# Kernel tuning notes

Measured on AMD Instinct MI355X. Metric: run time of the kernel, lower is better.

Reference implementation:

```python
import jax, jax.numpy as jnp
import numpy as np

N_NODES = 100000
N_EDGES = 1600000
HIDDEN = 64
N_MID = 3  # num_layers=5 -> 1 first + 3 middle + 1 last


def setup_inputs() -> dict:
    key = jax.random.key(0)
    ks = jax.random.split(key, 12)
    x = jax.random.normal(ks[0], (N_NODES, 1), dtype=jnp.float32)
    edge_index = jax.random.randint(ks[1], (2, N_EDGES), 0, N_NODES, dtype=jnp.int32)
    edge_weight = jax.random.uniform(ks[2], (N_EDGES,), dtype=jnp.float32)
    s0 = 1.0  # fan_in=1
    sh = 1.0 / np.sqrt(HIDDEN)
    Wrel0 = jax.random.normal(ks[3], (HIDDEN, 1), dtype=jnp.float32) * s0
    brel0 = jax.random.normal(ks[4], (HIDDEN,), dtype=jnp.float32) * s0
    Wroot0 = jax.random.normal(ks[5], (HIDDEN, 1), dtype=jnp.float32) * s0
    Wrel_mid = jax.random.normal(ks[6], (N_MID, HIDDEN, HIDDEN), dtype=jnp.float32) * sh
    brel_mid = jax.random.normal(ks[7], (N_MID, HIDDEN), dtype=jnp.float32) * sh
    Wroot_mid = jax.random.normal(ks[8], (N_MID, HIDDEN, HIDDEN), dtype=jnp.float32) * sh
    WrelL = jax.random.normal(ks[9], (1, HIDDEN), dtype=jnp.float32) * sh
    brelL = jax.random.normal(ks[10], (1,), dtype=jnp.float32) * sh
    WrootL = jax.random.normal(ks[11], (1, HIDDEN), dtype=jnp.float32) * sh
    return {"x": x, "edge_index": edge_index, "edge_weight": edge_weight,
            "Wrel0": Wrel0, "brel0": brel0, "Wroot0": Wroot0,
            "Wrel_mid": Wrel_mid, "brel_mid": brel_mid, "Wroot_mid": Wroot_mid,
            "WrelL": WrelL, "brelL": brelL, "WrootL": WrootL}


def reference(x, edge_index, edge_weight, Wrel0, brel0, Wroot0,
              Wrel_mid, brel_mid, Wroot_mid, WrelL, brelL, WrootL):
    src = edge_index[0]
    dst = edge_index[1]
    n = x.shape[0]

    def conv(h, Wrel, brel, Wroot):
        # PyG GraphConv(aggr='add'): lin_rel(sum_j w_ij * h_j) + lin_root(h_i)
        msg = h[src] * edge_weight[:, None]          # [E, C]
        agg = jax.ops.segment_sum(msg, dst, num_segments=n)  # [N, C]
        return agg @ Wrel.T + brel + h @ Wroot.T

    # dropout omitted (deterministic reference); relu after all but last layer
    h = jax.nn.relu(conv(x, Wrel0, brel0, Wroot0))
    for i in range(Wrel_mid.shape[0]):
        h = jax.nn.relu(conv(h, Wrel_mid[i], brel_mid[i], Wroot_mid[i]))
    return conv(h, WrelL, brelL, WrootL)  # [N, 1]
```

## Files before the change

kernel.cpp:

```cpp
#include <hip/hip_runtime.h>
#include <stdint.h>


#define NN 100000
#define NE 1600000
#define HID 64
#define NBKT 391
#define CAP 8192
#define TILE 4096
#define EPT 16
#define NTILE ((NE + TILE - 1) / TILE)
#define CHUNK 32

typedef __attribute__((ext_vector_type(8))) short bf16x8;
typedef __attribute__((ext_vector_type(4))) float f32x4;

__device__ __forceinline__ uint32_t rne_bf16(float v) {
    uint32_t u = __float_as_uint(v);
    return (u + 0x7fffu + ((u >> 16) & 1u)) >> 16;
}


__global__ __launch_bounds__(256) void k_bpart(const int* __restrict__ src,
                                               const int* __restrict__ dst,
                                               const float* __restrict__ w,
                                               int* __restrict__ bcur,
                                               int2* __restrict__ bpairs) {
    __shared__ int  hcnt[NBKT];
    __shared__ int  hoff[NBKT];
    __shared__ int  hadj[NBKT];
    __shared__ int  sc0[512];
    __shared__ int  sc1[512];
    __shared__ int2 sT[TILE];
    __shared__ int  sAdj[TILE];
    int tile0 = blockIdx.x * TILE;
    int t = threadIdx.x;
    for (int i = t; i < NBKT; i += 256) hcnt[i] = 0;
    __syncthreads();

    int   pk[EPT];
    int   bk[EPT];
    float wv[EPT];
    #pragma unroll
    for (int k = 0; k < EPT; k++) {
        int e = tile0 + t + k * 256;
        if (e < NE) {
            int d = dst[e];
            int b = d >> 8;
            pk[k] = (src[e] << 8) | (d & 255);
            wv[k] = w[e];
            bk[k] = b;
            atomicAdd(&hcnt[b], 1);
        } else {
            bk[k] = -1;
        }
    }
    __syncthreads();

    sc0[t]       = (t < NBKT) ? hcnt[t] : 0;
    sc0[t + 256] = (t + 256 < NBKT) ? hcnt[t + 256] : 0;
    __syncthreads();
    int* cur = sc0;
    int* oth = sc1;
    for (int off = 1; off < 512; off <<= 1) {
        int v0 = cur[t]       + ((t       >= off) ? cur[t - off]       : 0);
        int v1 = cur[t + 256] + ((t + 256 >= off) ? cur[t + 256 - off] : 0);
        oth[t] = v0;
        oth[t + 256] = v1;
        __syncthreads();
        int* tmp = cur; cur = oth; oth = tmp;
    }
    for (int i = t; i < NBKT; i += 256) {
        int c = hcnt[i];
        int excl = cur[i] - c;
        hoff[i] = excl;
        int gbase = c ? atomicAdd(&bcur[i], c) : 0;
        hadj[i] = gbase - excl;
        hcnt[i] = 0;
    }
    __syncthreads();

    #pragma unroll
    for (int k = 0; k < EPT; k++) {
        if (bk[k] >= 0) {
            int b = bk[k];
            int pos = hoff[b] + atomicAdd(&hcnt[b], 1);
            sT[pos] = make_int2(pk[k], __float_as_int(wv[k]));
            sAdj[pos] = hadj[b];
        }
    }
    __syncthreads();

    int n = NE - tile0; if (n > TILE) n = TILE;
    for (int j = t; j < n; j += 256)
        bpairs[sAdj[j] + j] = sT[j];
}

__global__ __launch_bounds__(256) void k_bcsr(const int* __restrict__ bcur,
                                              const int2* __restrict__ bpairs,
                                              int* __restrict__ offs,
                                              int* __restrict__ ends,
                                              uint32_t* __restrict__ pairs) {
    __shared__ int2 sE[CAP];
    __shared__ int cnt[256];
    __shared__ int scn[256];
    __shared__ int cur[256];
    int k = blockIdx.x, t = threadIdx.x;
    int base = k * CAP;
    int scnt = bcur[k] - base;
    cnt[t] = 0;
    __syncthreads();
    for (int j = t; j < scnt; j += 256) {
        int2 q = bpairs[base + j];
        sE[j] = q;
        atomicAdd(&cnt[q.x & 255], 1);
    }
    __syncthreads();
    int v = cnt[t], acc = v;
    scn[t] = v;
    __syncthreads();
    for (int off = 1; off < 256; off <<= 1) {
        int u = (t >= off) ? scn[t - off] : 0;
        __syncthreads();
        acc += u;
        scn[t] = acc;
        __syncthreads();
    }
    int excl = acc - v;
    cur[t] = excl;
    int d = (k << 8) + t;
    if (d < NN) {
        offs[d] = base + excl;
        ends[d] = base + excl + v;
    }
    __syncthreads();
    for (int j = t; j < scnt; j += 256) {
        int2 q = sE[j];
        int pos = base + atomicAdd(&cur[q.x & 255], 1);
        uint32_t wb = rne_bf16(__int_as_float(q.y)) & 0x7fffu;
        pairs[pos] = (wb << 17) | (uint32_t)(q.x >> 8);
    }
}


__global__ __launch_bounds__(256) void k_wsplit(const float* __restrict__ Wrel_mid,
                                                const float* __restrict__ Wroot_mid,
                                                uint16_t* __restrict__ WgH,
                                                uint16_t* __restrict__ WgL,
                                                uint16_t* __restrict__ WrH,
                                                uint16_t* __restrict__ WrL,
                                                int* __restrict__ bcur) {
    int i = blockIdx.x * blockDim.x + threadIdx.x;
    if (i < NBKT) bcur[i] = i * CAP;
    if (i >= 3 * 4096) return;
    float a = Wrel_mid[i];
    uint32_t ah = rne_bf16(a);
    float al = a - __uint_as_float(ah << 16);
    WgH[i] = (uint16_t)ah;
    WgL[i] = (uint16_t)rne_bf16(al);
    float b = Wroot_mid[i];
    uint32_t bh = rne_bf16(b);
    float bl = b - __uint_as_float(bh << 16);
    WrH[i] = (uint16_t)bh;
    WrL[i] = (uint16_t)rne_bf16(bl);
}


__device__ __forceinline__ void mfma_epilogue(
        int lane, int w, const uint32_t* sH,
        const uint16_t* __restrict__ WgH, const uint16_t* __restrict__ WgL,
        const uint16_t* __restrict__ WrH, const uint16_t* __restrict__ WrL,
        const float* __restrict__ brel,
        uint16_t* sG, uint16_t* sR) {
    int row = lane & 15;
    int quad = lane >> 4;
    int kb = quad * 8;
    bf16x8 ah0 = *(const bf16x8*)&sH[row * 36 + quad * 4];
    bf16x8 ah1 = *(const bf16x8*)&sH[row * 36 + 16 + quad * 4];
    int oc = w * 16 + row;
    {
        bf16x8 bh0 = *(const bf16x8*)&WgH[oc * 64 + kb];
        bf16x8 bh1 = *(const bf16x8*)&WgH[oc * 64 + 32 + kb];
        bf16x8 bl0 = *(const bf16x8*)&WgL[oc * 64 + kb];
        bf16x8 bl1 = *(const bf16x8*)&WgL[oc * 64 + 32 + kb];
        f32x4 acc = {0.f, 0.f, 0.f, 0.f};
        acc = __builtin_amdgcn_mfma_f32_16x16x32_bf16(ah0, bh0, acc, 0, 0, 0);
        acc = __builtin_amdgcn_mfma_f32_16x16x32_bf16(ah1, bh1, acc, 0, 0, 0);
        acc = __builtin_amdgcn_mfma_f32_16x16x32_bf16(ah0, bl0, acc, 0, 0, 0);
        acc = __builtin_amdgcn_mfma_f32_16x16x32_bf16(ah1, bl1, acc, 0, 0, 0);
        #pragma unroll
        for (int r = 0; r < 4; r++)
            sG[(quad * 4 + r) * 68 + oc] = (uint16_t)rne_bf16(acc[r]);
    }
    {
        bf16x8 bh0 = *(const bf16x8*)&WrH[oc * 64 + kb];
        bf16x8 bh1 = *(const bf16x8*)&WrH[oc * 64 + 32 + kb];
        bf16x8 bl0 = *(const bf16x8*)&WrL[oc * 64 + kb];
        bf16x8 bl1 = *(const bf16x8*)&WrL[oc * 64 + 32 + kb];
        float bias = brel[oc];
        f32x4 acc = {bias, bias, bias, bias};
        acc = __builtin_amdgcn_mfma_f32_16x16x32_bf16(ah0, bh0, acc, 0, 0, 0);
        acc = __builtin_amdgcn_mfma_f32_16x16x32_bf16(ah1, bh1, acc, 0, 0, 0);
        acc = __builtin_amdgcn_mfma_f32_16x16x32_bf16(ah0, bl0, acc, 0, 0, 0);
        acc = __builtin_amdgcn_mfma_f32_16x16x32_bf16(ah1, bl1, acc, 0, 0, 0);
        #pragma unroll
        for (int r = 0; r < 4; r++)
            sR[(quad * 4 + r) * 68 + oc] = (uint16_t)rne_bf16(acc[r]);
    }
}

__device__ __forceinline__ void epilogue_writeout(
        int tid, int blk16, const uint16_t* sG, const uint16_t* sR,
        uint16_t* __restrict__ Gout, uint16_t* __restrict__ Rout) {
    const uint32_t* sGd = (const uint32_t*)sG;
    const uint32_t* sRd = (const uint32_t*)sR;
    uint32_t* Gd = (uint32_t*)Gout;
    uint32_t* Rd = (uint32_t*)Rout;
    #pragma unroll
    for (int it = 0; it < 2; it++) {
        int idx = it * 256 + tid;
        int nd = idx >> 5, col = idx & 31;
        Gd[(blk16 + nd) * 32 + col] = sGd[nd * 34 + col];
        Rd[(blk16 + nd) * 32 + col] = sRd[nd * 34 + col];
    }
}


__global__ __launch_bounds__(256) void k_l0pre(
        const int* __restrict__ offs, const int* __restrict__ ends,
        const uint32_t* __restrict__ pairs, const float* __restrict__ x,
        const float* __restrict__ Wrel0, const float* __restrict__ brel0,
        const float* __restrict__ Wroot0,
        const uint16_t* __restrict__ WgH, const uint16_t* __restrict__ WgL,
        const uint16_t* __restrict__ WrH, const uint16_t* __restrict__ WrL,
        const float* __restrict__ brel,
        uint16_t* __restrict__ Gout, uint16_t* __restrict__ Rout) {
    __shared__ uint32_t sH[16 * 36];
    __shared__ uint16_t sG[16 * 68];
    __shared__ uint16_t sR[16 * 68];
    int c = threadIdx.x & 63;
    int w = threadIdx.x >> 6;
    int blk16 = blockIdx.x * 16;
    float agg[4];
    #pragma unroll
    for (int t = 0; t < 4; t++) {
        int node = blk16 + w * 4 + t;
        int b = offs[node], e = ends[node];
        float pp = 0.f;
        for (int j = b + c; j < e; j += 64) {
            uint32_t r = pairs[j];
            pp += __uint_as_float((r >> 17) << 16) * x[r & 0x1ffffu];
        }
        for (int o = 32; o > 0; o >>= 1) pp += __shfl_down(pp, o, 64);
        agg[t] = __shfl(pp, 0, 64);
    }
    float wr = Wrel0[c], br = brel0[c], wo = Wroot0[c];
    #pragma unroll
    for (int t = 0; t < 4; t++) {
        int node = blk16 + w * 4 + t;
        float v = agg[t] * wr + br + x[node] * wo;
        v = v > 0.f ? v : 0.f;
        uint32_t hb = rne_bf16(v);
        uint32_t pn = (uint32_t)__shfl_xor((int)hb, 1, 64);
        if (!(c & 1)) sH[(w * 4 + t) * 36 + (c >> 1)] = hb | (pn << 16);
    }
    __syncthreads();
    mfma_epilogue(c, w, sH, WgH, WgL, WrH, WrL, brel, sG, sR);
    __syncthreads();
    epilogue_writeout((int)threadIdx.x, blk16, sG, sR, Gout, Rout);
}

template <bool LAST>
__global__ __launch_bounds__(256, 4) void k_aggfused(
        const int* __restrict__ offs, const int* __restrict__ ends,
        const uint32_t* __restrict__ pairs,
        const uint16_t* __restrict__ Gb, const uint16_t* __restrict__ Rb,
        const uint16_t* __restrict__ WgH, const uint16_t* __restrict__ WgL,
        const uint16_t* __restrict__ WrH, const uint16_t* __restrict__ WrL,
        const float* __restrict__ brel,
        uint16_t* __restrict__ Gout, uint16_t* __restrict__ Rout,
        const float* __restrict__ WrelL, const float* __restrict__ WrootL,
        float* __restrict__ sarr, float* __restrict__ rarr) {
    __shared__ uint32_t sH[16 * 36];
    __shared__ uint16_t sG[16 * 68];
    __shared__ uint16_t sR[16 * 68];
    __shared__ __align__(128) uint16_t sStage[4][CHUNK * 64];
    int c = threadIdx.x & 63;
    int w = threadIdx.x >> 6;
    int blk16 = blockIdx.x * 16;
    int n0 = blk16 + w * 4;
    int ov = 0;
    if (c < 4) ov = offs[n0 + c];
    else if (c == 4) ov = ends[n0 + 3];
    int bnd[5];
    bnd[0] = __builtin_amdgcn_readlane(ov, 0);
    bnd[1] = __builtin_amdgcn_readlane(ov, 1);
    bnd[2] = __builtin_amdgcn_readlane(ov, 2);
    bnd[3] = __builtin_amdgcn_readlane(ov, 3);
    bnd[4] = __builtin_amdgcn_readlane(ov, 4);

    uint32_t ur[4];
    #pragma unroll
    for (int t = 0; t < 4; t++) ur[t] = Rb[(n0 + t) * 64 + c];

    float acc[4][4];
    #pragma unroll
    for (int t = 0; t < 4; t++)
        #pragma unroll
        for (int q = 0; q < 4; q++) acc[t][q] = 0.f;

    uint16_t* stg = sStage[w];
    const char* gbase = (const char*)Gb;
    int lg4   = (c >> 3) * 4;
    int lbyte = (c & 7) * 16;

    uint32_t p = 0;
    if (bnd[0] + c < bnd[4]) p = pairs[bnd[0] + c];

    for (int cb = bnd[0]; cb < bnd[4]; cb += 64) {
        uint32_t pn = 0;
        if (cb + 64 + c < bnd[4]) pn = pairs[cb + 64 + c];
        #pragma unroll
        for (int s = 0; s < 2; s++) {
            int sb = cb + s * 32;
            if (sb < bnd[4]) {
                int sn = bnd[4] - sb; if (sn > 32) sn = 32;
                int ni = (sn + 7) >> 3;
                #pragma unroll
                for (int i = 0; i < 4; i++) {
                    if (i < ni) {
                        int idx = (s * 32 + i * 8) * 4 + lg4;
                        uint32_t r = (uint32_t)__builtin_amdgcn_ds_bpermute(idx, (int)p);
                        uint32_t voff = ((r & 0x1ffffu) << 7) + (uint32_t)lbyte;
                        __builtin_amdgcn_global_load_lds(
                            (const __attribute__((address_space(1))) void*)(gbase + voff),
                            (__attribute__((address_space(3))) void*)((char*)stg + i * 1024),
                            16, 0, 0);
                    }
                }
                asm volatile("s_waitcnt vmcnt(0)" ::: "memory");
                #pragma unroll
                for (int t = 0; t < 4; t++) {
                    int lo = bnd[t] > sb ? bnd[t] : sb;
                    int hi = bnd[t + 1] < sb + sn ? bnd[t + 1] : sb + sn;
                    int j = lo;
                    for (; j + 8 <= hi; j += 8) {
                        uint32_t rr[8], gg[8];
                        #pragma unroll
                        for (int q = 0; q < 8; q++)
                            rr[q] = __builtin_amdgcn_readlane(p, j - cb + q);
                        #pragma unroll
                        for (int q = 0; q < 8; q++)
                            gg[q] = (uint32_t)stg[(j - sb + q) * 64 + c];
                        #pragma unroll
                        for (int q = 0; q < 8; q++)
                            acc[t][q & 3] += __uint_as_float((rr[q] >> 17) << 16)
                                           * __uint_as_float(gg[q] << 16);
                    }
                    for (; j + 4 <= hi; j += 4) {
                        uint32_t rr[4], gg[4];
                        #pragma unroll
                        for (int q = 0; q < 4; q++)
                            rr[q] = __builtin_amdgcn_readlane(p, j - cb + q);
                        #pragma unroll
                        for (int q = 0; q < 4; q++)
                            gg[q] = (uint32_t)stg[(j - sb + q) * 64 + c];
                        #pragma unroll
                        for (int q = 0; q < 4; q++)
                            acc[t][q] += __uint_as_float((rr[q] >> 17) << 16)
                                       * __uint_as_float(gg[q] << 16);
                    }
                    for (; j < hi; j++) {
                        uint32_t r = __builtin_amdgcn_readlane(p, j - cb);
                        uint32_t g = (uint32_t)stg[(j - sb) * 64 + c];
                        acc[t][0] += __uint_as_float((r >> 17) << 16)
                                   * __uint_as_float(g << 16);
                    }
                }
            }
        }
        p = pn;
    }

    #pragma unroll
    for (int t = 0; t < 4; t++) {
        float v = (acc[t][0] + acc[t][1]) + (acc[t][2] + acc[t][3])
                + __uint_as_float(ur[t] << 16);
        v = v > 0.f ? v : 0.f;
        if (!LAST) {
            uint32_t hb = rne_bf16(v);
            uint32_t pn2 = (uint32_t)__shfl_xor((int)hb, 1, 64);
            if (!(c & 1)) sH[(w * 4 + t) * 36 + (c >> 1)] = hb | (pn2 << 16);
        } else {
            float a = v * WrelL[c];
            float r = v * WrootL[c];
            for (int o = 32; o > 0; o >>= 1) {
                a += __shfl_down(a, o, 64);
                r += __shfl_down(r, o, 64);
            }
            if (c == 0) { sarr[n0 + t] = a; rarr[n0 + t] = r; }
        }
    }
    if (!LAST) {
        __syncthreads();
        mfma_epilogue(c, w, sH, WgH, WgL, WrH, WrL, brel, sG, sR);
        __syncthreads();
        epilogue_writeout((int)threadIdx.x, blk16, sG, sR, Gout, Rout);
    }
}

__global__ void k_last(const int* __restrict__ offs, const int* __restrict__ ends,
                       const uint32_t* __restrict__ pairs,
                       const float* __restrict__ sarr, const float* __restrict__ rarr,
                       const float* __restrict__ brelL, float* __restrict__ out) {
    int i = blockIdx.x * blockDim.x + threadIdx.x;
    if (i >= NN) return;
    float a0 = rarr[i] + brelL[0], a1 = 0.f;
    int b = offs[i], e = ends[i];
    int j = b;
    for (; j + 2 <= e; j += 2) {
        uint32_t r0 = pairs[j], r1 = pairs[j + 1];
        a0 += __uint_as_float((r0 >> 17) << 16) * sarr[r0 & 0x1ffffu];
        a1 += __uint_as_float((r1 >> 17) << 16) * sarr[r1 & 0x1ffffu];
    }
    for (; j < e; j++) {
        uint32_t r = pairs[j];
        a0 += __uint_as_float((r >> 17) << 16) * sarr[r & 0x1ffffu];
    }
    out[i] = a0 + a1;
}

extern "C" void kernel_launch(void* const* d_in, const int* in_sizes, int n_in,
                              void* d_out, int out_size, void* d_ws, size_t ws_size,
                              hipStream_t stream) {
    const float* x        = (const float*)d_in[0];
    const int*   ei       = (const int*)d_in[1];
    const float* ew       = (const float*)d_in[2];
    const float* Wrel0    = (const float*)d_in[3];
    const float* brel0    = (const float*)d_in[4];
    const float* Wroot0   = (const float*)d_in[5];
    const float* Wrel_mid = (const float*)d_in[6];
    const float* brel_mid = (const float*)d_in[7];
    const float* Wroot_mid= (const float*)d_in[8];
    const float* WrelL    = (const float*)d_in[9];
    const float* brelL    = (const float*)d_in[10];
    const float* WrootL   = (const float*)d_in[11];
    float* out = (float*)d_out;

    const int* src  = ei;
    const int* dstp = ei + NE;

    char* w = (char*)d_ws;
    size_t o = 0;
    auto alloc = [&](size_t b) -> void* {
        void* r = (void*)(w + o);
        o += (b + 255) & ~(size_t)255;
        return r;
    };
    int*      offs  = (int*)alloc((size_t)NN * 4);
    int*      ends  = (int*)alloc((size_t)NN * 4);
    int*      bcur  = (int*)alloc((size_t)NBKT * 4);
    uint16_t* WgH   = (uint16_t*)alloc((size_t)3 * 4096 * 2);
    uint16_t* WgL   = (uint16_t*)alloc((size_t)3 * 4096 * 2);
    uint16_t* WrH   = (uint16_t*)alloc((size_t)3 * 4096 * 2);
    uint16_t* WrL   = (uint16_t*)alloc((size_t)3 * 4096 * 2);
    float*    sarr  = (float*)alloc((size_t)NN * 4);
    float*    rarr  = (float*)alloc((size_t)NN * 4);
    uint32_t* pairs = (uint32_t*)alloc((size_t)NBKT * CAP * 4);
    uint16_t* GbA   = (uint16_t*)alloc((size_t)NN * HID * 2);
    uint16_t* RbA   = (uint16_t*)alloc((size_t)NN * HID * 2);
    uint16_t* GbB   = (uint16_t*)alloc((size_t)NN * HID * 2);
    uint16_t* RbB   = (uint16_t*)alloc((size_t)NN * HID * 2);
    (void)RbB;
    int2*  bpairs = (int2*)GbB;

    k_wsplit<<<(3 * 4096 + 255) / 256, 256, 0, stream>>>(
        Wrel_mid, Wroot_mid, WgH, WgL, WrH, WrL, bcur);

    k_bpart<<<NTILE, 256, 0, stream>>>(src, dstp, ew, bcur, bpairs);
    k_bcsr<<<NBKT, 256, 0, stream>>>(bcur, bpairs, offs, ends, pairs);

    k_l0pre<<<NN / 16, 256, 0, stream>>>(
        offs, ends, pairs, x, Wrel0, brel0, Wroot0,
        WgH, WgL, WrH, WrL, brel_mid, GbA, RbA);

    k_aggfused<false><<<NN / 16, 256, 0, stream>>>(
        offs, ends, pairs, GbA, RbA,
        WgH + 4096, WgL + 4096, WrH + 4096, WrL + 4096, brel_mid + HID,
        GbB, RbB, WrelL, WrootL, sarr, rarr);
    k_aggfused<false><<<NN / 16, 256, 0, stream>>>(
        offs, ends, pairs, GbB, RbB,
        WgH + 2 * 4096, WgL + 2 * 4096, WrH + 2 * 4096, WrL + 2 * 4096,
        brel_mid + 2 * HID, GbA, RbA, WrelL, WrootL, sarr, rarr);
    k_aggfused<true><<<NN / 16, 256, 0, stream>>>(
        offs, ends, pairs, GbA, RbA,
        WgH, WgL, WrH, WrL, brel_mid,
        GbB, RbB, WrelL, WrootL, sarr, rarr);

    k_last<<<(NN + 255) / 256, 256, 0, stream>>>(offs, ends, pairs, sarr, rarr, brelL, out);
}
```

Baseline: 311.0 us.

## Compute edge aggregation with MFMA using transposed LDS reads and masked weight rows

Replaces the scalar per-edge readlane/FMA accumulation in the fused aggregation kernel with 16x16x32 bf16 MFMA. Edge weights form a masked A matrix, one row per destination node, and the gathered neighbor features are read from LDS with ds_read_b64_tr_b16 as the B operand. The root term is preloaded into the accumulators. LDS is consolidated into a single reused buffer and launch bounds are raised to 6 blocks per CU for more occupancy. The MFMA wastes 12 of 16 rows, and the new gather layout and transpose reads add LDS traffic and complexity.

```diff
diff --git a/kernel.cpp b/kernel.cpp
--- a/kernel.cpp
+++ b/kernel.cpp
@@ -10,10 +10,11 @@
 #define TILE 4096
 #define EPT 16
 #define NTILE ((NE + TILE - 1) / TILE)
-#define CHUNK 32
 
 typedef __attribute__((ext_vector_type(8))) short bf16x8;
 typedef __attribute__((ext_vector_type(4))) float f32x4;
+typedef __attribute__((ext_vector_type(2))) unsigned int u32x2;
+typedef __attribute__((ext_vector_type(4))) unsigned int u32x4;
 
 __device__ __forceinline__ uint32_t rne_bf16(float v) {
     uint32_t u = __float_as_uint(v);
@@ -270,8 +271,12 @@
     epilogue_writeout((int)threadIdx.x, blk16, sG, sR, Gout, Rout);
 }
 
+#define TRR(dst, off) \
+    asm volatile("ds_read_b64_tr_b16 %0, %1 offset:" #off \
+                 : "=v"(dst) : "v"(trb))
+
 template <bool LAST>
-__global__ __launch_bounds__(256, 4) void k_aggfused(
+__global__ __launch_bounds__(256, 6) void k_aggfused(
         const int* __restrict__ offs, const int* __restrict__ ends,
         const uint32_t* __restrict__ pairs,
         const uint16_t* __restrict__ Gb, const uint16_t* __restrict__ Rb,
@@ -282,9 +287,7 @@
         const float* __restrict__ WrelL, const float* __restrict__ WrootL,
         float* __restrict__ sarr, float* __restrict__ rarr) {
     __shared__ uint32_t sH[16 * 36];
-    __shared__ uint16_t sG[16 * 68];
-    __shared__ uint16_t sR[16 * 68];
-    __shared__ __align__(128) uint16_t sStage[4][CHUNK * 64];
+    __shared__ __align__(128) char smem[16384];
     int c = threadIdx.x & 63;
     int w = threadIdx.x >> 6;
     int blk16 = blockIdx.x * 16;
@@ -299,113 +302,158 @@
     bnd[3] = __builtin_amdgcn_readlane(ov, 3);
     bnd[4] = __builtin_amdgcn_readlane(ov, 4);
 
-    uint32_t ur[4];
-    #pragma unroll
-    for (int t = 0; t < 4; t++) ur[t] = Rb[(n0 + t) * 64 + c];
-
-    float acc[4][4];
-    #pragma unroll
-    for (int t = 0; t < 4; t++)
-        #pragma unroll
-        for (int q = 0; q < 4; q++) acc[t][q] = 0.f;
-
-    uint16_t* stg = sStage[w];
+    int arow  = c & 15;
+    int kq    = (c >> 4) * 8;
+    int eprm  = ((c >> 5) << 2) | ((c >> 1) & 3);
+    int lbyte = ((c >> 3) & 3) * 32 + (c & 1) * 16;
+    char* stg = smem + w * 4096;
+    uint32_t stgOff = (uint32_t)(uintptr_t)
+        (__attribute__((address_space(3))) char*)stg;
+    uint32_t trb = stgOff + ((uint32_t)(c >> 4) << 10)
+                          + ((uint32_t)(c & 15) << 3);
+
+    int blo = bnd[0], bhi = bnd[1];
+    if (arow == 1) { blo = bnd[1]; bhi = bnd[2]; }
+    if (arow == 2) { blo = bnd[2]; bhi = bnd[3]; }
+    if (arow == 3) { blo = bnd[3]; bhi = bnd[4]; }
+    if (arow >= 4) { blo = 0;      bhi = 0;      }
+    uint32_t wid = (uint32_t)(bhi - blo);
+
+    {
+        f32x4 z = {0.f, 0.f, 0.f, 0.f};
+        #pragma unroll
+        for (int i = 0; i < 4; i++)
+            *(f32x4*)(stg + i * 1024 + c * 16) = z;
+        asm volatile("s_waitcnt lgkmcnt(0)" ::: "memory");
+    }
+
+    f32x4 acc16[4];
+    {
+        int ur[4];
+        #pragma unroll
+        for (int t = 0; t < 4; t++) ur[t] = (int)(uint32_t)Rb[(n0 + t) * 64 + c];
+        #pragma unroll
+        for (int nb = 0; nb < 4; nb++) {
+            int idx = (nb * 16 + (c & 15)) * 4;
+            f32x4 ci;
+            #pragma unroll
+            for (int t = 0; t < 4; t++) {
+                uint32_t rv = (uint32_t)__builtin_amdgcn_ds_bpermute(idx, ur[t]);
+                ci[t] = __uint_as_float(rv << 16);
+            }
+            acc16[nb] = ci;
+        }
+    }
+
     const char* gbase = (const char*)Gb;
-    int lg4   = (c >> 3) * 4;
-    int lbyte = (c & 7) * 16;
-
     uint32_t p = 0;
     if (bnd[0] + c < bnd[4]) p = pairs[bnd[0] + c];
 
     for (int cb = bnd[0]; cb < bnd[4]; cb += 64) {
-        uint32_t pn = 0;
-        if (cb + 64 + c < bnd[4]) pn = pairs[cb + 64 + c];
+        uint32_t pnext = 0;
+        if (cb + 64 + c < bnd[4]) pnext = pairs[cb + 64 + c];
         #pragma unroll
         for (int s = 0; s < 2; s++) {
             int sb = cb + s * 32;
             if (sb < bnd[4]) {
                 int sn = bnd[4] - sb; if (sn > 32) sn = 32;
                 int ni = (sn + 7) >> 3;
+                int es4 = (s * 32 + eprm) * 4;
                 #pragma unroll
                 for (int i = 0; i < 4; i++) {
                     if (i < ni) {
-                        int idx = (s * 32 + i * 8) * 4 + lg4;
-                        uint32_t r = (uint32_t)__builtin_amdgcn_ds_bpermute(idx, (int)p);
+                        uint32_t r = (uint32_t)__builtin_amdgcn_ds_bpermute(
+                            es4 + i * 32, (int)p);
                         uint32_t voff = ((r & 0x1ffffu) << 7) + (uint32_t)lbyte;
                         __builtin_amdgcn_global_load_lds(
                             (const __attribute__((address_space(1))) void*)(gbase + voff),
-                            (__attribute__((address_space(3))) void*)((char*)stg + i * 1024),
+                            (__attribute__((address_space(3))) void*)(stg + i * 1024),
                             16, 0, 0);
                     }
                 }
                 asm volatile("s_waitcnt vmcnt(0)" ::: "memory");
+                u32x2 tb0, tb1, tb2, tb3, tb4, tb5, tb6, tb7;
+                TRR(tb0, 0);   TRR(tb1, 512);
+                TRR(tb2, 128); TRR(tb3, 640);
+                TRR(tb4, 256); TRR(tb5, 768);
+                TRR(tb6, 384); TRR(tb7, 896);
+                int kidx = s * 128 + kq * 4;
+                int db = sb + kq - blo;
+                uint32_t m[8];
                 #pragma unroll
-                for (int t = 0; t < 4; t++) {
-                    int lo = bnd[t] > sb ? bnd[t] : sb;
-                    int hi = bnd[t + 1] < sb + sn ? bnd[t + 1] : sb + sn;
-                    int j = lo;
-                    for (; j + 8 <= hi; j += 8) {
-                        uint32_t rr[8], gg[8];
-                        #pragma unroll
-                        for (int q = 0; q < 8; q++)
-                            rr[q] = __builtin_amdgcn_readlane(p, j - cb + q);
-                        #pragma unroll
-                        for (int q = 0; q < 8; q++)
-                            gg[q] = (uint32_t)stg[(j - sb + q) * 64 + c];
-                        #pragma unroll
-                        for (int q = 0; q < 8; q++)
-                            acc[t][q & 3] += __uint_as_float((rr[q] >> 17) << 16)
-                                           * __uint_as_float(gg[q] << 16);
-                    }
-                    for (; j + 4 <= hi; j += 4) {
-                        uint32_t rr[4], gg[4];
-                        #pragma unroll
-                        for (int q = 0; q < 4; q++)
-                            rr[q] = __builtin_amdgcn_readlane(p, j - cb + q);
-                        #pragma unroll
-                        for (int q = 0; q < 4; q++)
-                            gg[q] = (uint32_t)stg[(j - sb + q) * 64 + c];
-                        #pragma unroll
-                        for (int q = 0; q < 4; q++)
-                            acc[t][q] += __uint_as_float((rr[q] >> 17) << 16)
-                                       * __uint_as_float(gg[q] << 16);
-                    }
-                    for (; j < hi; j++) {
-                        uint32_t r = __builtin_amdgcn_readlane(p, j - cb);
-                        uint32_t g = (uint32_t)stg[(j - sb) * 64 + c];
-                        acc[t][0] += __uint_as_float((r >> 17) << 16)
-                                   * __uint_as_float(g << 16);
-                    }
+                for (int q = 0; q < 8; q++) {
+                    uint32_t rq = (uint32_t)__builtin_amdgcn_ds_bpermute(
+                        kidx + q * 4, (int)p);
+                    uint32_t bf = rq >> 17;
+                    m[q] = ((uint32_t)(db + q) < wid) ? bf : 0u;
+                }
+                u32x4 aa = { m[0] | (m[1] << 16), m[2] | (m[3] << 16),
+                             m[4] | (m[5] << 16), m[6] | (m[7] << 16) };
+                bf16x8 af = __builtin_bit_cast(bf16x8, aa);
+                asm volatile("s_waitcnt lgkmcnt(0)" ::: "memory");
+                __builtin_amdgcn_sched_barrier(0);
+                {
+                    u32x4 bb0 = { tb0.x, tb0.y, tb1.x, tb1.y };
+                    acc16[0] = __builtin_amdgcn_mfma_f32_16x16x32_bf16(
+                        af, __builtin_bit_cast(bf16x8, bb0), acc16[0], 0, 0, 0);
+                    u32x4 bb1 = { tb2.x, tb2.y, tb3.x, tb3.y };
+                    acc16[1] = __builtin_amdgcn_mfma_f32_16x16x32_bf16(
+                        af, __builtin_bit_cast(bf16x8, bb1), acc16[1], 0, 0, 0);
+                    u32x4 bb2 = { tb4.x, tb4.y, tb5.x, tb5.y };
+                    acc16[2] = __builtin_amdgcn_mfma_f32_16x16x32_bf16(
+                        af, __builtin_bit_cast(bf16x8, bb2), acc16[2], 0, 0, 0);
+                    u32x4 bb3 = { tb6.x, tb6.y, tb7.x, tb7.y };
+                    acc16[3] = __builtin_amdgcn_mfma_f32_16x16x32_bf16(
+                        af, __builtin_bit_cast(bf16x8, bb3), acc16[3], 0, 0, 0);
                 }
             }
         }
-        p = pn;
-    }
-
-    #pragma unroll
-    for (int t = 0; t < 4; t++) {
-        float v = (acc[t][0] + acc[t][1]) + (acc[t][2] + acc[t][3])
-                + __uint_as_float(ur[t] << 16);
-        v = v > 0.f ? v : 0.f;
-        if (!LAST) {
-            uint32_t hb = rne_bf16(v);
-            uint32_t pn2 = (uint32_t)__shfl_xor((int)hb, 1, 64);
-            if (!(c & 1)) sH[(w * 4 + t) * 36 + (c >> 1)] = hb | (pn2 << 16);
-        } else {
-            float a = v * WrelL[c];
-            float r = v * WrootL[c];
-            for (int o = 32; o > 0; o >>= 1) {
-                a += __shfl_down(a, o, 64);
-                r += __shfl_down(r, o, 64);
+        p = pnext;
+    }
+
+    if (!LAST) {
+        #pragma unroll
+        for (int t = 0; t < 4; t++) {
+            #pragma unroll
+            for (int nb = 0; nb < 4; nb++) {
+                float v = acc16[nb][t];
+                v = v > 0.f ? v : 0.f;
+                uint32_t hb = rne_bf16(v);
+                uint32_t pn2 = (uint32_t)__shfl_xor((int)hb, 1, 64);
+                if (!(c & 1) && c < 16)
+                    sH[(w * 4 + t) * 36 + nb * 8 + (c >> 1)] = hb | (pn2 << 16);
             }
-            if (c == 0) { sarr[n0 + t] = a; rarr[n0 + t] = r; }
-        }
-    }
-    if (!LAST) {
+        }
         __syncthreads();
+        uint16_t* sG = (uint16_t*)smem;
+        uint16_t* sR = (uint16_t*)(smem + 2176);
         mfma_epilogue(c, w, sH, WgH, WgL, WrH, WrL, brel, sG, sR);
         __syncthreads();
         epilogue_writeout((int)threadIdx.x, blk16, sG, sR, Gout, Rout);
+    } else {
+        float wl[4], wo[4];
+        #pragma unroll
+        for (int nb = 0; nb < 4; nb++) {
+            wl[nb] = WrelL[nb * 16 + (c & 15)];
+            wo[nb] = WrootL[nb * 16 + (c & 15)];
+        }
+        #pragma unroll
+        for (int t = 0; t < 4; t++) {
+            float pa = 0.f, pr = 0.f;
+            #pragma unroll
+            for (int nb = 0; nb < 4; nb++) {
+                float v = acc16[nb][t];
+                v = v > 0.f ? v : 0.f;
+                pa += v * wl[nb];
+                pr += v * wo[nb];
+            }
+            #pragma unroll
+            for (int o = 8; o > 0; o >>= 1) {
+                pa += __shfl_down(pa, o, 64);
+                pr += __shfl_down(pr, o, 64);
+            }
+            if (c == 0) { sarr[n0 + t] = pa; rarr[n0 + t] = pr; }
+        }
     }
 }
 
```

After: 319.9 us. 2.9% more time.
